# Kernel tuning notes

Measured on AMD Instinct MI355X. Metric: run time of the kernel, lower is better.

Reference implementation:

```python
import jax, jax.numpy as jnp
import numpy as np

MIN_TAU = 1e-3  # max(1e-5, config.CELL_MIN_TAU=0.001)
EPS_U = 1e-10   # guard for log(u) in gumbel transform


def setup_inputs() -> dict:
    key = jax.random.key(0)
    ks = jax.random.split(key, 6)
    B, I, H = 16, 1024, 2048
    x_t = jax.random.normal(ks[0], (B, I), dtype=jnp.float32)
    h_prev = jax.random.normal(ks[1], (B, H), dtype=jnp.float32)
    W_ih_w = jax.random.normal(ks[2], (H, I), dtype=jnp.float32) * (1.0 / np.sqrt(I))
    W_ih_b = jax.random.normal(ks[3], (H,), dtype=jnp.float32) * 0.01
    W_hh = jax.random.normal(ks[4], (H, H), dtype=jnp.float32) * np.sqrt(2.0 / (H + H))  # xavier
    hh_mask = jnp.ones((H, H), dtype=jnp.float32)
    temperature = jnp.ones((1,), dtype=jnp.float32)
    gumbel_noise = jax.random.uniform(ks[5], (B, H, H), dtype=jnp.float32)  # U(0,1); transformed in reference
    return {"x_t": x_t, "h_prev": h_prev, "W_ih_w": W_ih_w, "W_ih_b": W_ih_b,
            "W_hh": W_hh, "hh_mask": hh_mask, "temperature": temperature,
            "gumbel_noise": gumbel_noise}


def reference(x_t, h_prev, W_ih_w, W_ih_b, W_hh, hh_mask, temperature, gumbel_noise):
    # tau = clamp(temperature, min=1e-3)
    tau = jnp.maximum(temperature[0], MIN_TAU)
    # input contribution: Linear(input_size, hidden_size)
    input_contrib = x_t @ W_ih_w.T + W_ih_b  # (B, H)
    # effective recurrent logits (H, H), broadcast over batch
    effective = (W_hh * hh_mask) / tau
    # gumbel-softmax with tau=1.0, soft (training mode): softmax(logits + g) over last dim
    g = -jnp.log(-jnp.log(gumbel_noise + EPS_U) + EPS_U)  # standard Gumbel(0,1)
    gumbel_samples = jax.nn.softmax(effective[None, :, :] + g, axis=2)  # (B, H, H)
    # contrib = einsum('boh,bh->bo')
    contrib = jnp.einsum('boh,bh->bo', gumbel_samples, h_prev)
    preact = input_contrib + contrib
    # default neuron plan: single tanh kernel over all hidden units
    h_next = jnp.tanh(preact)
    return h_next
```

## Files before the change

kernel.cpp:

```cpp
#include <hip/hip_runtime.h>
#include <math.h>

#define BB 16
#define II 1024
#define HH 2048

__device__ __forceinline__ float gumbel_xf(float u) {
    float l1 = __logf(u + 1e-10f);
    return -__logf(-l1 + 1e-10f);
}

__global__ __launch_bounds__(256, 4) void reservoir_cell_kernel(
    const float* __restrict__ x_t,
    const float* __restrict__ h_prev,
    const float* __restrict__ W_ih_w,
    const float* __restrict__ W_ih_b,
    const float* __restrict__ W_hh,
    const float* __restrict__ hh_mask,
    const float* __restrict__ temperature,
    const float* __restrict__ gumbel,
    float* __restrict__ out)
{
    const int n    = blockIdx.x;
    const int o    = ((n >> 5) << 3) + (n & 7);
    const int grp  = (n >> 3) & 3;
    const int wave = threadIdx.x >> 6;
    const int lane = threadIdx.x & 63;
    const int b    = (grp << 2) + wave;

    const float tau     = fmaxf(temperature[0], 1e-3f);
    const float inv_tau = 1.0f / tau;

    const float4* x4 = (const float4*)(x_t + (size_t)b * II);
    const float4* w4 = (const float4*)(W_ih_w + (size_t)o * II);
    float ic = 0.0f;
    #pragma unroll
    for (int j = 0; j < 4; ++j) {
        float4 xv = x4[j * 64 + lane];
        float4 wv = w4[j * 64 + lane];
        ic += xv.x * wv.x + xv.y * wv.y + xv.z * wv.z + xv.w * wv.w;
    }

    const float4* g4 = (const float4*)(gumbel + ((size_t)b * HH + o) * HH);
    const float4* h4 = (const float4*)(W_hh   + (size_t)o * HH);
    const float4* m4 = (const float4*)(hh_mask+ (size_t)o * HH);
    const float4* p4 = (const float4*)(h_prev + (size_t)b * HH);

    float s = 0.0f, t = 0.0f;
    #pragma unroll 4
    for (int j = 0; j < 8; ++j) {
        float4 u  = g4[j * 64 + lane];
        float4 w  = h4[j * 64 + lane];
        float4 mk = m4[j * 64 + lane];
        float4 hv = p4[j * 64 + lane];
        float e;
        e = __expf(w.x * mk.x * inv_tau + gumbel_xf(u.x)); s += e; t += e * hv.x;
        e = __expf(w.y * mk.y * inv_tau + gumbel_xf(u.y)); s += e; t += e * hv.y;
        e = __expf(w.z * mk.z * inv_tau + gumbel_xf(u.z)); s += e; t += e * hv.z;
        e = __expf(w.w * mk.w * inv_tau + gumbel_xf(u.w)); s += e; t += e * hv.w;
    }

    #pragma unroll
    for (int off = 32; off; off >>= 1) {
        ic += __shfl_down(ic, off, 64);
        s  += __shfl_down(s,  off, 64);
        t  += __shfl_down(t,  off, 64);
    }

    if (lane == 0) {
        out[(size_t)b * HH + o] = tanhf(ic + W_ih_b[o] + t / s);
    }
}

extern "C" void kernel_launch(void* const* d_in, const int* in_sizes, int n_in,
                              void* d_out, int out_size, void* d_ws, size_t ws_size,
                              hipStream_t stream) {
    const float* x_t         = (const float*)d_in[0];
    const float* h_prev      = (const float*)d_in[1];
    const float* W_ih_w      = (const float*)d_in[2];
    const float* W_ih_b      = (const float*)d_in[3];
    const float* W_hh        = (const float*)d_in[4];
    const float* hh_mask     = (const float*)d_in[5];
    const float* temperature = (const float*)d_in[6];
    const float* gumbel      = (const float*)d_in[7];
    float* out = (float*)d_out;

    dim3 grid(8192), block(256);
    reservoir_cell_kernel<<<grid, block, 0, stream>>>(
        x_t, h_prev, W_ih_w, W_ih_b, W_hh, hh_mask, temperature, gumbel, out);
}
```

Measured before the change: 411.7 us.

## Precompute exp of scaled recurrent logits and fold Gumbel into reciprocal

Uses the identity exp(a - log(-log u)) = exp(a) / (-log u) to replace one log and one exp per element with a reciprocal. A new prepass kernel computes exp(W_hh*mask/tau) once into workspace, so the main kernel reads a single matrix instead of W_hh and hh_mask. This cuts transcendental work and memory traffic per element, at the cost of an extra launch and a write of a 16 MB intermediate. Computing exp without subtracting a max could overflow if tau is small, though softmax normalisation otherwise keeps the result the same.

```diff
diff --git a/kernel.cpp b/kernel.cpp
--- a/kernel.cpp
+++ b/kernel.cpp
@@ -5,9 +5,23 @@
 #define II 1024
 #define HH 2048
 
-__device__ __forceinline__ float gumbel_xf(float u) {
-    float l1 = __logf(u + 1e-10f);
-    return -__logf(-l1 + 1e-10f);
+__global__ __launch_bounds__(256) void precompute_q_kernel(
+    const float* __restrict__ W_hh,
+    const float* __restrict__ hh_mask,
+    const float* __restrict__ temperature,
+    float* __restrict__ Q)
+{
+    const float tau = fmaxf(temperature[0], 1e-3f);
+    const float inv_tau = 1.0f / tau;
+    const int idx = blockIdx.x * blockDim.x + threadIdx.x;
+    float4 w  = ((const float4*)W_hh)[idx];
+    float4 mk = ((const float4*)hh_mask)[idx];
+    float4 q;
+    q.x = __expf(w.x * mk.x * inv_tau);
+    q.y = __expf(w.y * mk.y * inv_tau);
+    q.z = __expf(w.z * mk.z * inv_tau);
+    q.w = __expf(w.w * mk.w * inv_tau);
+    ((float4*)Q)[idx] = q;
 }
 
 __global__ __launch_bounds__(256, 4) void reservoir_cell_kernel(
@@ -15,9 +29,7 @@
     const float* __restrict__ h_prev,
     const float* __restrict__ W_ih_w,
     const float* __restrict__ W_ih_b,
-    const float* __restrict__ W_hh,
-    const float* __restrict__ hh_mask,
-    const float* __restrict__ temperature,
+    const float* __restrict__ Q,
     const float* __restrict__ gumbel,
     float* __restrict__ out)
 {
@@ -27,9 +39,6 @@
     const int wave = threadIdx.x >> 6;
     const int lane = threadIdx.x & 63;
     const int b    = (grp << 2) + wave;
-
-    const float tau     = fmaxf(temperature[0], 1e-3f);
-    const float inv_tau = 1.0f / tau;
 
     const float4* x4 = (const float4*)(x_t + (size_t)b * II);
     const float4* w4 = (const float4*)(W_ih_w + (size_t)o * II);
@@ -42,22 +51,20 @@
     }
 
     const float4* g4 = (const float4*)(gumbel + ((size_t)b * HH + o) * HH);
-    const float4* h4 = (const float4*)(W_hh   + (size_t)o * HH);
-    const float4* m4 = (const float4*)(hh_mask+ (size_t)o * HH);
+    const float4* q4 = (const float4*)(Q      + (size_t)o * HH);
     const float4* p4 = (const float4*)(h_prev + (size_t)b * HH);
 
     float s = 0.0f, t = 0.0f;
     #pragma unroll 4
     for (int j = 0; j < 8; ++j) {
         float4 u  = g4[j * 64 + lane];
-        float4 w  = h4[j * 64 + lane];
-        float4 mk = m4[j * 64 + lane];
+        float4 qv = q4[j * 64 + lane];
         float4 hv = p4[j * 64 + lane];
-        float e;
-        e = __expf(w.x * mk.x * inv_tau + gumbel_xf(u.x)); s += e; t += e * hv.x;
-        e = __expf(w.y * mk.y * inv_tau + gumbel_xf(u.y)); s += e; t += e * hv.y;
-        e = __expf(w.z * mk.z * inv_tau + gumbel_xf(u.z)); s += e; t += e * hv.z;
-        e = __expf(w.w * mk.w * inv_tau + gumbel_xf(u.w)); s += e; t += e * hv.w;
+        float L, e;
+        L = 1e-10f - __logf(u.x + 1e-10f); e = qv.x * __builtin_amdgcn_rcpf(L); s += e; t += e * hv.x;
+        L = 1e-10f - __logf(u.y + 1e-10f); e = qv.y * __builtin_amdgcn_rcpf(L); s += e; t += e * hv.y;
+        L = 1e-10f - __logf(u.z + 1e-10f); e = qv.z * __builtin_amdgcn_rcpf(L); s += e; t += e * hv.z;
+        L = 1e-10f - __logf(u.w + 1e-10f); e = qv.w * __builtin_amdgcn_rcpf(L); s += e; t += e * hv.w;
     }
 
     #pragma unroll
@@ -84,8 +91,11 @@
     const float* temperature = (const float*)d_in[6];
     const float* gumbel      = (const float*)d_in[7];
     float* out = (float*)d_out;
+    float* Q   = (float*)d_ws;
 
-    dim3 grid(8192), block(256);
-    reservoir_cell_kernel<<<grid, block, 0, stream>>>(
-        x_t, h_prev, W_ih_w, W_ih_b, W_hh, hh_mask, temperature, gumbel, out);
+    precompute_q_kernel<<<dim3(HH * HH / 4 / 256), dim3(256), 0, stream>>>(
+        W_hh, hh_mask, temperature, Q);
+
+    reservoir_cell_kernel<<<dim3(8192), dim3(256), 0, stream>>>(
+        x_t, h_prev, W_ih_w, W_ih_b, Q, gumbel, out);
 }
```

Result: no change. 408.9 us (-0.7%).

## Factor gumbel softmax exponent into precomputed exp(W) times reciprocal of log term

Applied to the files above, without the earlier changes.

Rewrites exp(w/tau - log(-log u)) as exp(w/tau) * 1/(-log u). This drops one log and the exp from the per-element inner loop over the large gumbel tensor, leaving one log and a hardware reciprocal. Each block now owns one output row and loops over all 16 batches, so the exp(W_hh row) factors and the W_ih row load are computed once and reused from registers. The grid shrinks to 2048 blocks and register pressure rises from the cached rows. The epsilon handling differs slightly from the reference, and the approximate reciprocal may change numerics.

```diff
diff --git a/kernel.cpp b/kernel.cpp
--- a/kernel.cpp
+++ b/kernel.cpp
@@ -4,11 +4,6 @@
 #define BB 16
 #define II 1024
 #define HH 2048
-
-__device__ __forceinline__ float gumbel_xf(float u) {
-    float l1 = __logf(u + 1e-10f);
-    return -__logf(-l1 + 1e-10f);
-}
 
 __global__ __launch_bounds__(256, 4) void reservoir_cell_kernel(
     const float* __restrict__ x_t,
@@ -21,54 +16,68 @@
     const float* __restrict__ gumbel,
     float* __restrict__ out)
 {
-    const int n    = blockIdx.x;
-    const int o    = ((n >> 5) << 3) + (n & 7);
-    const int grp  = (n >> 3) & 3;
+    const int o    = blockIdx.x;
     const int wave = threadIdx.x >> 6;
     const int lane = threadIdx.x & 63;
-    const int b    = (grp << 2) + wave;
 
     const float tau     = fmaxf(temperature[0], 1e-3f);
     const float inv_tau = 1.0f / tau;
 
-    const float4* x4 = (const float4*)(x_t + (size_t)b * II);
-    const float4* w4 = (const float4*)(W_ih_w + (size_t)o * II);
-    float ic = 0.0f;
+    const float4* wh4 = (const float4*)(W_hh   + (size_t)o * HH);
+    const float4* mk4 = (const float4*)(hh_mask+ (size_t)o * HH);
+    float4 Q[8];
     #pragma unroll
-    for (int j = 0; j < 4; ++j) {
-        float4 xv = x4[j * 64 + lane];
-        float4 wv = w4[j * 64 + lane];
-        ic += xv.x * wv.x + xv.y * wv.y + xv.z * wv.z + xv.w * wv.w;
+    for (int j = 0; j < 8; ++j) {
+        float4 w = wh4[j * 64 + lane];
+        float4 m = mk4[j * 64 + lane];
+        Q[j].x = __expf(w.x * m.x * inv_tau);
+        Q[j].y = __expf(w.y * m.y * inv_tau);
+        Q[j].z = __expf(w.z * m.z * inv_tau);
+        Q[j].w = __expf(w.w * m.w * inv_tau);
     }
+    const float4* wi4 = (const float4*)(W_ih_w + (size_t)o * II);
+    float4 Wi[4];
+    #pragma unroll
+    for (int j = 0; j < 4; ++j) Wi[j] = wi4[j * 64 + lane];
 
-    const float4* g4 = (const float4*)(gumbel + ((size_t)b * HH + o) * HH);
-    const float4* h4 = (const float4*)(W_hh   + (size_t)o * HH);
-    const float4* m4 = (const float4*)(hh_mask+ (size_t)o * HH);
-    const float4* p4 = (const float4*)(h_prev + (size_t)b * HH);
+    const float bias = W_ih_b[o];
 
-    float s = 0.0f, t = 0.0f;
-    #pragma unroll 4
-    for (int j = 0; j < 8; ++j) {
-        float4 u  = g4[j * 64 + lane];
-        float4 w  = h4[j * 64 + lane];
-        float4 mk = m4[j * 64 + lane];
-        float4 hv = p4[j * 64 + lane];
-        float e;
-        e = __expf(w.x * mk.x * inv_tau + gumbel_xf(u.x)); s += e; t += e * hv.x;
-        e = __expf(w.y * mk.y * inv_tau + gumbel_xf(u.y)); s += e; t += e * hv.y;
-        e = __expf(w.z * mk.z * inv_tau + gumbel_xf(u.z)); s += e; t += e * hv.z;
-        e = __expf(w.w * mk.w * inv_tau + gumbel_xf(u.w)); s += e; t += e * hv.w;
-    }
+    #pragma unroll 1
+    for (int i = 0; i < 4; ++i) {
+        const int b = (i << 2) + wave;
 
-    #pragma unroll
-    for (int off = 32; off; off >>= 1) {
-        ic += __shfl_down(ic, off, 64);
-        s  += __shfl_down(s,  off, 64);
-        t  += __shfl_down(t,  off, 64);
-    }
+        const float4* x4 = (const float4*)(x_t + (size_t)b * II);
+        float ic = 0.0f;
+        #pragma unroll
+        for (int j = 0; j < 4; ++j) {
+            float4 xv = x4[j * 64 + lane];
+            ic += xv.x * Wi[j].x + xv.y * Wi[j].y + xv.z * Wi[j].z + xv.w * Wi[j].w;
+        }
 
-    if (lane == 0) {
-        out[(size_t)b * HH + o] = tanhf(ic + W_ih_b[o] + t / s);
+        const float4* g4 = (const float4*)(gumbel + ((size_t)b * HH + o) * HH);
+        const float4* p4 = (const float4*)(h_prev + (size_t)b * HH);
+        float s = 0.0f, t = 0.0f;
+        #pragma unroll 4
+        for (int j = 0; j < 8; ++j) {
+            float4 u  = g4[j * 64 + lane];
+            float4 hv = p4[j * 64 + lane];
+            float L, e;
+            L = 1e-10f - __logf(u.x + 1e-10f); e = Q[j].x * __builtin_amdgcn_rcpf(L); s += e; t += e * hv.x;
+            L = 1e-10f - __logf(u.y + 1e-10f); e = Q[j].y * __builtin_amdgcn_rcpf(L); s += e; t += e * hv.y;
+            L = 1e-10f - __logf(u.z + 1e-10f); e = Q[j].z * __builtin_amdgcn_rcpf(L); s += e; t += e * hv.z;
+            L = 1e-10f - __logf(u.w + 1e-10f); e = Q[j].w * __builtin_amdgcn_rcpf(L); s += e; t += e * hv.w;
+        }
+
+        #pragma unroll
+        for (int off = 32; off; off >>= 1) {
+            ic += __shfl_down(ic, off, 64);
+            s  += __shfl_down(s,  off, 64);
+            t  += __shfl_down(t,  off, 64);
+        }
+
+        if (lane == 0) {
+            out[(size_t)b * HH + o] = tanhf(ic + bias + t / s);
+        }
     }
 }
 
@@ -85,7 +94,6 @@
     const float* gumbel      = (const float*)d_in[7];
     float* out = (float*)d_out;
 
-    dim3 grid(8192), block(256);
-    reservoir_cell_kernel<<<grid, block, 0, stream>>>(
+    reservoir_cell_kernel<<<dim3(HH), dim3(256), 0, stream>>>(
         x_t, h_prev, W_ih_w, W_ih_b, W_hh, hh_mask, temperature, gumbel, out);
 }
```

Result: slower. 423.4 us (+2.8%).
